# Performance work log

Measured on AMD Instinct MI355X. Metric: run time of the kernel, lower is better.

The kernel has to match this reference:

```python
import jax, jax.numpy as jnp
import numpy as np
import math

B, T, C = 4, 1024, 1024
H = 16          # n_head
E = 8           # num_experts
K = 2           # top_k
HID = 4096      # expert_hidden_dim
TEMP = 1.0
EPS_LN = 1e-5


def setup_inputs() -> dict:
    key = jax.random.key(0)
    ks = jax.random.split(key, 16)
    s = 0.02
    return {
        'x': jax.random.normal(ks[0], (B, T, C), jnp.float32),
        'ln1_g': jnp.ones((C,), jnp.float32),
        'ln1_b': jnp.zeros((C,), jnp.float32),
        'W_qkv': jax.random.normal(ks[1], (C, 3 * C), jnp.float32) * s,
        'b_qkv': jnp.zeros((3 * C,), jnp.float32),
        'W_proj': jax.random.normal(ks[2], (C, C), jnp.float32) * s,
        'b_proj': jnp.zeros((C,), jnp.float32),
        'ln2_g': jnp.ones((C,), jnp.float32),
        'ln2_b': jnp.zeros((C,), jnp.float32),
        'W_router': jax.random.normal(ks[3], (C, E), jnp.float32) * s,
        'W1': jax.random.normal(ks[4], (E, C, HID), jnp.float32) * s,
        'b1': jnp.zeros((E, HID), jnp.float32),
        'W2': jax.random.normal(ks[5], (E, HID, C), jnp.float32) * s,
        'b2': jnp.zeros((E, C), jnp.float32),
    }


def _layernorm(x, g, b):
    mu = jnp.mean(x, axis=-1, keepdims=True)
    var = jnp.mean(jnp.square(x - mu), axis=-1, keepdims=True)
    return (x - mu) * jax.lax.rsqrt(var + EPS_LN) * g + b


def reference(x, ln1_g, ln1_b, W_qkv, b_qkv, W_proj, b_proj,
              ln2_g, ln2_b, W_router, W1, b1, W2, b2):
    D = C // H
    # --- causal self-attention on ln_1(x) ---
    h = _layernorm(x, ln1_g, ln1_b)
    qkv = h @ W_qkv + b_qkv                      # [B,T,3C]
    q, k, v = jnp.split(qkv, 3, axis=-1)
    q = q.reshape(B, T, H, D).transpose(0, 2, 1, 3)   # [B,H,T,D]
    k = k.reshape(B, T, H, D).transpose(0, 2, 1, 3)
    v = v.reshape(B, T, H, D).transpose(0, 2, 1, 3)
    att = jnp.einsum('bhqd,bhkd->bhqk', q, k) * (1.0 / math.sqrt(D))
    mask = jnp.tril(jnp.ones((T, T), bool))
    att = jnp.where(mask, att, -jnp.inf)
    att = jax.nn.softmax(att, axis=-1)
    y = jnp.einsum('bhqk,bhkd->bhqd', att, v)
    y = y.transpose(0, 2, 1, 3).reshape(B, T, C)
    x = x + (y @ W_proj + b_proj)

    # --- sparse MoE on ln_2(x) ---
    h2 = _layernorm(x, ln2_g, ln2_b)
    xf = h2.reshape(-1, C)                       # [N,C]
    N = xf.shape[0]
    logits = (xf @ W_router) / TEMP              # [N,E]
    prob = jax.nn.softmax(logits, axis=-1)
    top_prob, top_idx = jax.lax.top_k(prob, K)   # [N,K]
    top_prob = top_prob / (jnp.sum(top_prob, axis=-1, keepdims=True) + 1e-9)
    # dense per-token per-expert combine weights (0 for unselected experts)
    w = jnp.zeros((N, E), xf.dtype).at[jnp.arange(N)[:, None], top_idx].add(top_prob)
    # dense expert compute (weights zero out unselected experts -> same math)
    hid = jax.nn.gelu(jnp.einsum('nc,ech->neh', xf, W1) + b1, approximate=False)
    eo = jnp.einsum('neh,ehc->nec', hid, W2) + b2          # [N,E,C]
    out_flat = jnp.einsum('nec,ne->nc', eo, w)
    x = x + out_flat.reshape(B, T, C)

    counts = jnp.zeros((E,), jnp.float32).at[top_idx.reshape(-1)].add(1.0)
    expert_utilization = counts / (jnp.sum(counts) + 1e-9)
    return x, expert_utilization
```

## Files before the change

kernel.cpp:

```cpp
#include <hip/hip_runtime.h>
#include <cmath>

#define CDIM 1024
#define NTOK 4096
#define NHEAD 16
#define HDIM 64
#define NEXP 8
#define HIDD 4096
#define MAXROWS 9216

typedef short bf16x8 __attribute__((ext_vector_type(8)));
typedef short s16x4  __attribute__((ext_vector_type(4)));
typedef float f32x4  __attribute__((ext_vector_type(4)));

static __device__ __forceinline__ short f2bf(float f){
  unsigned u = __builtin_bit_cast(unsigned, f);
  u += 0x7fffu + ((u >> 16) & 1u);
  return (short)(u >> 16);
}
static __device__ __forceinline__ float bf2f(short s){
  unsigned u = ((unsigned)(unsigned short)s) << 16;
  return __builtin_bit_cast(float, u);
}

static __device__ __forceinline__ int swz64(int r, int ch){
  return r*64 + (((ch ^ (r>>1)) & 3) << 4);
}
static __device__ __forceinline__ int swz128(int r, int ch){
  return r*128 + (((ch ^ r) & 7) << 4);
}

static __device__ __forceinline__ void gl16(const short* g, short* l){
  __builtin_amdgcn_global_load_lds(
      (const __attribute__((address_space(1))) void*)g,
      (__attribute__((address_space(3))) void*)l, 16, 0, 0);
}

__global__ void k_transpose_cast(const float* __restrict__ in, short* __restrict__ out,
                                 int R, int Cc){
  __shared__ float tile[64][65];
  const int z = blockIdx.z;
  const float* src = in + (long long)z*R*Cc;
  short* dst = out + (long long)z*R*Cc;
  const int r0 = blockIdx.y*64, c0 = blockIdx.x*64;
  const int t = threadIdx.x;
  #pragma unroll
  for (int it=0; it<4; ++it){
    const int item = t + it*256;
    const int r = item>>4, c4 = item&15;
    const float4 v = *(const float4*)(src + (long long)(r0+r)*Cc + c0 + c4*4);
    tile[r][c4*4+0]=v.x; tile[r][c4*4+1]=v.y; tile[r][c4*4+2]=v.z; tile[r][c4*4+3]=v.w;
  }
  __syncthreads();
  #pragma unroll
  for (int it=0; it<2; ++it){
    const int item = t + it*256;
    const int rr8 = item & 7, cc = item >> 3;
    bf16x8 o;
    #pragma unroll
    for (int i=0;i<8;i++) o[i] = f2bf(tile[rr8*8+i][cc]);
    *(bf16x8*)(dst + (long long)(c0+cc)*R + r0 + rr8*8) = o;
  }
}

__global__ void k_ln1(const float* __restrict__ x, const float* __restrict__ g,
                      const float* __restrict__ b, short* __restrict__ out){
  const int row = blockIdx.x;
  const int t = threadIdx.x;
  const float4 v = ((const float4*)(x + (long long)row*CDIM))[t];
  float s  = v.x+v.y+v.z+v.w;
  float s2 = v.x*v.x+v.y*v.y+v.z*v.z+v.w*v.w;
  #pragma unroll
  for (int mm=1; mm<64; mm<<=1){ s += __shfl_xor(s,mm); s2 += __shfl_xor(s2,mm); }
  __shared__ float ps[4], ps2[4];
  const int w = t>>6, l = t&63;
  if (l==0){ ps[w]=s; ps2[w]=s2; }
  __syncthreads();
  s  = ps[0]+ps[1]+ps[2]+ps[3];
  s2 = ps2[0]+ps2[1]+ps2[2]+ps2[3];
  const float mu = s*(1.f/CDIM);
  const float rstd = rsqrtf(s2*(1.f/CDIM) - mu*mu + 1e-5f);
  const float4 gg = ((const float4*)g)[t];
  const float4 bb = ((const float4*)b)[t];
  s16x4 o;
  o[0]=f2bf((v.x-mu)*rstd*gg.x+bb.x); o[1]=f2bf((v.y-mu)*rstd*gg.y+bb.y);
  o[2]=f2bf((v.z-mu)*rstd*gg.z+bb.z); o[3]=f2bf((v.w-mu)*rstd*gg.w+bb.w);
  *(s16x4*)(out + (long long)row*CDIM + t*4) = o;
}

__global__ void k_ln2_router(const float* __restrict__ x1, const float* __restrict__ g,
                             const float* __restrict__ b, const float* __restrict__ Wr,
                             short* __restrict__ h2, int* __restrict__ tidx,
                             float* __restrict__ tw, int* __restrict__ counts){
  const int row = blockIdx.x;
  const int t = threadIdx.x;
  const float4 v = ((const float4*)(x1 + (long long)row*CDIM))[t];
  float s  = v.x+v.y+v.z+v.w;
  float s2 = v.x*v.x+v.y*v.y+v.z*v.z+v.w*v.w;
  #pragma unroll
  for (int mm=1; mm<64; mm<<=1){ s += __shfl_xor(s,mm); s2 += __shfl_xor(s2,mm); }
  __shared__ float ps[4], ps2[4];
  const int w = t>>6, l = t&63;
  if (l==0){ ps[w]=s; ps2[w]=s2; }
  __syncthreads();
  s  = ps[0]+ps[1]+ps[2]+ps[3];
  s2 = ps2[0]+ps2[1]+ps2[2]+ps2[3];
  const float mu = s*(1.f/CDIM);
  const float rstd = rsqrtf(s2*(1.f/CDIM) - mu*mu + 1e-5f);
  const float4 gg = ((const float4*)g)[t];
  const float4 bb = ((const float4*)b)[t];
  const float y0=(v.x-mu)*rstd*gg.x+bb.x, y1=(v.y-mu)*rstd*gg.y+bb.y;
  const float y2=(v.z-mu)*rstd*gg.z+bb.z, y3=(v.w-mu)*rstd*gg.w+bb.w;
  s16x4 o; o[0]=f2bf(y0); o[1]=f2bf(y1); o[2]=f2bf(y2); o[3]=f2bf(y3);
  *(s16x4*)(h2 + (long long)row*CDIM + t*4) = o;

  float acc[8];
  const float* wr0 = Wr + (long long)(t*4)*NEXP;
  #pragma unroll
  for (int e=0;e<8;e++) acc[e] = y0*wr0[e] + y1*wr0[8+e] + y2*wr0[16+e] + y3*wr0[24+e];
  #pragma unroll
  for (int mm=1; mm<64; mm<<=1){
    #pragma unroll
    for (int e=0;e<8;e++) acc[e] += __shfl_xor(acc[e], mm);
  }
  __shared__ float pl[4][8];
  if (l==0){
    #pragma unroll
    for (int e=0;e<8;e++) pl[w][e]=acc[e];
  }
  __syncthreads();
  if (t==0){
    float lg[8];
    #pragma unroll
    for (int e=0;e<8;e++) lg[e] = pl[0][e]+pl[1][e]+pl[2][e]+pl[3][e];
    float mx = lg[0];
    #pragma unroll
    for (int e=1;e<8;e++) mx = fmaxf(mx, lg[e]);
    float pr[8]; float sum = 0.f;
    #pragma unroll
    for (int e=0;e<8;e++){ pr[e]=expf(lg[e]-mx); sum += pr[e]; }
    int i0 = 0;
    #pragma unroll
    for (int e=1;e<8;e++) if (pr[e] > pr[i0]) i0 = e;
    int i1 = (i0==0) ? 1 : 0;
    #pragma unroll
    for (int e=0;e<8;e++) if (e!=i0 && pr[e] > pr[i1]) i1 = e;
    const float p0 = pr[i0]/sum, p1 = pr[i1]/sum;
    const float dn = p0 + p1 + 1e-9f;
    tidx[row*2]=i0; tidx[row*2+1]=i1;
    tw[row*2]=p0/dn; tw[row*2+1]=p1/dn;
    atomicAdd(&counts[i0],1); atomicAdd(&counts[i1],1);
  }
}

__global__ void k_route_setup(const int* __restrict__ counts, int* __restrict__ offs,
                              int* __restrict__ cursors, float* __restrict__ util){
  if (threadIdx.x == 0){
    int o = 0;
    for (int e=0;e<8;e++){
      offs[e] = o; cursors[e] = o;
      o += (counts[e] + 127) & ~127;
    }
    offs[8] = o;
    for (int e=0;e<8;e++) util[e] = (float)counts[e] / 8192.0f;
  }
}

__global__ void k_scatter(const int* __restrict__ tidx, const float* __restrict__ tw,
                          int* __restrict__ cursors, int* __restrict__ rowmap,
                          float* __restrict__ roww, int* __restrict__ posmap){
  const int i = blockIdx.x*blockDim.x + threadIdx.x;
  if (i >= 2*NTOK) return;
  const int e = tidx[i];
  const int pos = atomicAdd(&cursors[e], 1);
  rowmap[pos] = i >> 1;
  roww[pos]   = tw[i];
  posmap[i]   = pos;
}

template<int EPI>
__launch_bounds__(512, 4)
__global__ void k_gemm(const short* __restrict__ A, const short* __restrict__ Bt,
                       const float* __restrict__ bias, const float* __restrict__ resid,
                       void* __restrict__ Cout, int N, int K,
                       const int* __restrict__ rowmap, const int* __restrict__ offs,
                       long long expStrideB, const short* __restrict__ zrow){
  int wg = blockIdx.x;
  const int nwg = gridDim.x;
  {
    const int q = nwg >> 3, r8 = nwg & 7;
    const int xcd = wg & 7, pos = wg >> 3;
    wg = (xcd < r8 ? xcd*(q+1) : r8*(q+1) + (xcd - r8)*q) + pos;
  }
  const int gridN = N >> 7;
  const int gridM = nwg / gridN;
  const int mtile = wg % gridM, ntile = wg / gridM;
  const int mbase = mtile*128;
  const int nbase = ntile*128;
  int e = 0;
  if constexpr (EPI >= 2){
    if (mbase >= offs[8]) return;
    while (e < 7 && mbase >= offs[e+1]) e++;
    Bt += (long long)e * expStrideB;
  }
  __shared__ short Asm[2][4096];
  __shared__ short Bsm[2][4096];
  const int tid = threadIdx.x;
  const int w = tid >> 6, l = tid & 63;
  const int wr = w >> 1, wc = w & 1;
  const int l15 = l & 15, l4 = l >> 4;

  const short* aSrc; const short* bSrc;
  {
    const int r = tid >> 2, ch = tid & 3;
    const int sch = (ch ^ (r >> 1)) & 3;
    if constexpr (EPI == 2){
      const int grow = rowmap[mbase + r];
      aSrc = (grow >= 0) ? (A + (long long)grow*K + sch*8) : (zrow + sch*8);
    } else {
      aSrc = A + (long long)(mbase + r)*K + sch*8;
    }
    bSrc = Bt + (long long)(nbase + r)*K + sch*8;
  }
  const int dOff = w*512;

  f32x4 acc[2][4];
  const f32x4 z4 = {0.f,0.f,0.f,0.f};
  #pragma unroll
  for (int i=0;i<2;i++){
    #pragma unroll
    for (int jn=0;jn<4;jn++) acc[i][jn] = z4;
  }

  auto stage = [&](int buf, int kt){
    gl16(aSrc + kt, &Asm[buf][dOff]);
    gl16(bSrc + kt, &Bsm[buf][dOff]);
  };
  auto compute = [&](int buf){
    bf16x8 af[2], bfr[4];
    #pragma unroll
    for (int i=0;i<2;i++)
      af[i]  = *(const bf16x8*)((char*)Asm[buf] + swz64(wr*32 + i*16 + l15, l4));
    #pragma unroll
    for (int jn=0;jn<4;jn++)
      bfr[jn] = *(const bf16x8*)((char*)Bsm[buf] + swz64(wc*64 + jn*16 + l15, l4));
    #pragma unroll
    for (int i=0;i<2;i++){
      #pragma unroll
      for (int jn=0;jn<4;jn++)
        acc[i][jn] = __builtin_amdgcn_mfma_f32_16x16x32_bf16(af[i], bfr[jn], acc[i][jn], 0,0,0);
    }
  };

  stage(0, 0);
  asm volatile("s_waitcnt vmcnt(0)" ::: "memory");
  __builtin_amdgcn_s_barrier();

  int cur = 0;
  for (int kt = 32; kt < K; kt += 32){
    stage(cur ^ 1, kt);
    compute(cur);
    asm volatile("s_waitcnt vmcnt(0)" ::: "memory");
    __builtin_amdgcn_s_barrier();
    cur ^= 1;
  }
  compute(cur);

  #pragma unroll
  for (int i=0;i<2;i++){
    const int row0 = mbase + wr*32 + i*16 + l4*4;
    #pragma unroll
    for (int jn=0;jn<4;jn++){
      const int col = nbase + wc*64 + jn*16 + l15;
      const float bi = bias[(EPI>=2 ? e*N : 0) + col];
      #pragma unroll
      for (int j=0;j<4;j++){
        const long long idx = (long long)(row0 + j)*N + col;
        float v = acc[i][jn][j] + bi;
        if constexpr (EPI == 0){
          ((short*)Cout)[idx] = f2bf(v);
        } else if constexpr (EPI == 1){
          ((float*)Cout)[idx] = v + resid[idx];
        } else if constexpr (EPI == 2){
          ((short*)Cout)[idx] = f2bf(0.5f*v*(1.0f + erff(v*0.70710678118654752f)));
        } else {
          ((short*)Cout)[idx] = f2bf(v);
        }
      }
    }
  }
}

__launch_bounds__(512)
__global__ void k_attn(const short* __restrict__ qkv, short* __restrict__ y){
  const int qp = blockIdx.x;
  const int bh = blockIdx.y;
  const int bb = bh >> 4;
  const int h  = bh & 15;
  const int tid = threadIdx.x;
  const int w = tid >> 6, l = tid & 63;
  const int half = w >> 2, wq = w & 3;
  const int l15 = l & 15, l4 = l >> 4;

  __shared__ short Ksm[64*64];
  __shared__ short Vtsm[64*64];
  __shared__ short Psm[8*16*64];

  const long long rs = 3*CDIM;
  const int qrow0 = bb*1024 + qp*128;
  const int myQt = (qp << 1) + half;
  const int qtHigh = (qp << 1) + 1;

  bf16x8 aq[2];
  {
    const int qr = qrow0 + half*64 + wq*16 + l15;
    const short* qp2 = qkv + (long long)qr*rs + h*HDIM;
    aq[0] = *(const bf16x8*)(qp2 + l4*8);
    aq[1] = *(const bf16x8*)(qp2 + 32 + l4*8);
  }

  const f32x4 z4 = {0.f,0.f,0.f,0.f};
  f32x4 O[4];
  #pragma unroll
  for (int cf=0;cf<4;cf++) O[cf] = z4;
  float mrow[4], lrow[4];
  #pragma unroll
  for (int j=0;j<4;j++){ mrow[j] = -1e30f; lrow[j] = 0.f; }

  for (int kvb = 0; kvb <= qtHigh; ++kvb){
    const int kvrow0 = bb*1024 + kvb*64;
    {
      const int r = tid >> 3, c = tid & 7;
      const short* kp = qkv + (long long)(kvrow0 + r)*rs + CDIM + h*HDIM + c*8;
      *(bf16x8*)((char*)Ksm + swz128(r, c)) = *(const bf16x8*)kp;
      const short* vp = qkv + (long long)(kvrow0 + r)*rs + 2*CDIM + h*HDIM + c*8;
      bf16x8 vv = *(const bf16x8*)vp;
      const int off2 = 2*r;
      const int g0 = off2 >> 4, b0 = off2 & 15;
      #pragma unroll
      for (int i=0;i<8;i++){
        const int d = c*8 + i;
        *(short*)((char*)Vtsm + d*128 + (((g0 ^ d) & 7) << 4) + b0) = vv[i];
      }
    }
    __syncthreads();

    if (kvb <= myQt){
      f32x4 S[4];
      #pragma unroll
      for (int cf=0;cf<4;cf++) S[cf] = z4;
      #pragma unroll
      for (int cf=0;cf<4;cf++){
        #pragma unroll
        for (int kf=0;kf<2;kf++){
          bf16x8 bk = *(const bf16x8*)((char*)Ksm + swz128(cf*16 + l15, kf*4 + l4));
          S[cf] = __builtin_amdgcn_mfma_f32_16x16x32_bf16(aq[kf], bk, S[cf], 0,0,0);
        }
      }

      const bool diag = (kvb == myQt);
      #pragma unroll
      for (int cf=0;cf<4;cf++){
        #pragma unroll
        for (int j=0;j<4;j++){
          float s = S[cf][j] * 0.125f;
          if (diag && (cf*16 + l15 > wq*16 + l4*4 + j)) s = -1e30f;
          S[cf][j] = s;
        }
      }

      float alpha[4];
      #pragma unroll
      for (int j=0;j<4;j++){
        float mx = fmaxf(fmaxf(S[0][j],S[1][j]), fmaxf(S[2][j],S[3][j]));
        #pragma unroll
        for (int mm=1; mm<16; mm<<=1) mx = fmaxf(mx, __shfl_xor(mx, mm));
        const float mnew = fmaxf(mrow[j], mx);
        const float al = expf(mrow[j] - mnew);
        float psum = 0.f;
        #pragma unroll
        for (int cf=0;cf<4;cf++){ float pp = expf(S[cf][j]-mnew); S[cf][j]=pp; psum += pp; }
        #pragma unroll
        for (int mm=1; mm<16; mm<<=1) psum += __shfl_xor(psum, mm);
        lrow[j] = lrow[j]*al + psum;
        mrow[j] = mnew; alpha[j] = al;
      }
      #pragma unroll
      for (int cf=0;cf<4;cf++){
        #pragma unroll
        for (int j=0;j<4;j++) O[cf][j] *= alpha[j];
      }

      char* pw = (char*)Psm + w*2048;
      #pragma unroll
      for (int cf=0;cf<4;cf++){
        #pragma unroll
        for (int j=0;j<4;j++){
          const int r = l4*4 + j;
          const int cb = (cf*16 + l15)*2;
          *(short*)(pw + r*128 + ((((cb>>4) ^ r) & 7)<<4) + (cb & 15)) = f2bf(S[cf][j]);
        }
      }
      bf16x8 pa[2];
      pa[0] = *(const bf16x8*)(pw + swz128(l15, l4));
      pa[1] = *(const bf16x8*)(pw + swz128(l15, 4 + l4));
      #pragma unroll
      for (int cf=0;cf<4;cf++){
        #pragma unroll
        for (int kf=0;kf<2;kf++){
          bf16x8 bv = *(const bf16x8*)((char*)Vtsm + swz128(cf*16 + l15, kf*4 + l4));
          O[cf] = __builtin_amdgcn_mfma_f32_16x16x32_bf16(pa[kf], bv, O[cf], 0,0,0);
        }
      }
    }
    __syncthreads();
  }

  const int yr0 = qrow0 + half*64 + wq*16;
  #pragma unroll
  for (int cf=0;cf<4;cf++){
    #pragma unroll
    for (int j=0;j<4;j++){
      const int r = l4*4 + j;
      y[(long long)(yr0 + r)*CDIM + h*HDIM + cf*16 + l15] = f2bf(O[cf][j] / lrow[j]);
    }
  }
}

__global__ void k_combine(const float* __restrict__ x1, const short* __restrict__ eo,
                          const int* __restrict__ posmap, const float* __restrict__ roww,
                          float* __restrict__ out){
  const int row = blockIdx.x;
  const int t = threadIdx.x;
  const int p0 = posmap[row*2], p1 = posmap[row*2+1];
  const float w0 = roww[p0], w1 = roww[p1];
  const float4 a  = ((const float4*)(x1 + (long long)row*CDIM))[t];
  const s16x4 e0 = *(const s16x4*)(eo + (long long)p0*CDIM + t*4);
  const s16x4 e1 = *(const s16x4*)(eo + (long long)p1*CDIM + t*4);
  float4 r;
  r.x = a.x + w0*bf2f(e0[0]) + w1*bf2f(e1[0]);
  r.y = a.y + w0*bf2f(e0[1]) + w1*bf2f(e1[1]);
  r.z = a.z + w0*bf2f(e0[2]) + w1*bf2f(e1[2]);
  r.w = a.w + w0*bf2f(e0[3]) + w1*bf2f(e1[3]);
  ((float4*)(out + (long long)row*CDIM))[t] = r;
}

extern "C" void kernel_launch(void* const* d_in, const int* in_sizes, int n_in,
                              void* d_out, int out_size, void* d_ws, size_t ws_size,
                              hipStream_t stream){
  const float* x     = (const float*)d_in[0];
  const float* ln1_g = (const float*)d_in[1];
  const float* ln1_b = (const float*)d_in[2];
  const float* W_qkv = (const float*)d_in[3];
  const float* b_qkv = (const float*)d_in[4];
  const float* W_proj= (const float*)d_in[5];
  const float* b_proj= (const float*)d_in[6];
  const float* ln2_g = (const float*)d_in[7];
  const float* ln2_b = (const float*)d_in[8];
  const float* W_r   = (const float*)d_in[9];
  const float* W1    = (const float*)d_in[10];
  const float* b1    = (const float*)d_in[11];
  const float* W2    = (const float*)d_in[12];
  const float* b2    = (const float*)d_in[13];
  float* out = (float*)d_out;
  float* util = out + (long long)NTOK*CDIM;

  char* p = (char*)d_ws;
  auto alloc = [&](size_t bytes)->char*{
    char* r = p; p += (bytes + 255) & ~(size_t)255; return r;
  };
  short* Wt1   = (short*)alloc((size_t)NEXP*HIDD*CDIM*2);
  short* Wt2   = (short*)alloc((size_t)NEXP*CDIM*HIDD*2);
  float* x1    = (float*)alloc((size_t)NTOK*CDIM*4);
  short* h2    = (short*)alloc((size_t)NTOK*CDIM*2);
  short* hid   = (short*)alloc((size_t)MAXROWS*HIDD*2);
  int*   tidx  = (int*)alloc(2*NTOK*4);
  float* tw    = (float*)alloc(2*NTOK*4);
  int*   counts= (int*)alloc(256);
  int*   offs  = (int*)alloc(256);
  int*   curs  = (int*)alloc(256);
  int*   rowmap= (int*)alloc(MAXROWS*4);
  float* roww  = (float*)alloc(MAXROWS*4);
  int*   posmap= (int*)alloc(2*NTOK*4);
  short* zrow  = (short*)alloc(8192);
  char* transStart = p;
  short* WtQ = (short*)alloc((size_t)3*CDIM*CDIM*2);
  short* WtP = (short*)alloc((size_t)CDIM*CDIM*2);
  short* h   = (short*)alloc((size_t)NTOK*CDIM*2);
  short* qkv = (short*)alloc((size_t)NTOK*3*CDIM*2);
  short* y   = (short*)alloc((size_t)NTOK*CDIM*2);
  short* eo  = (short*)transStart;

  (void)hipMemsetAsync(counts, 0, 32, stream);
  (void)hipMemsetAsync(zrow, 0, 8192, stream);
  (void)hipMemsetAsync(rowmap, 0xFF, MAXROWS*4, stream);

  k_transpose_cast<<<dim3(3*CDIM/64, CDIM/64, 1), 256, 0, stream>>>(W_qkv, WtQ, CDIM, 3*CDIM);
  k_transpose_cast<<<dim3(CDIM/64, CDIM/64, 1),   256, 0, stream>>>(W_proj, WtP, CDIM, CDIM);
  k_transpose_cast<<<dim3(HIDD/64, CDIM/64, NEXP),256, 0, stream>>>(W1, Wt1, CDIM, HIDD);
  k_transpose_cast<<<dim3(CDIM/64, HIDD/64, NEXP),256, 0, stream>>>(W2, Wt2, HIDD, CDIM);

  k_ln1<<<NTOK, 256, 0, stream>>>(x, ln1_g, ln1_b, h);

  k_gemm<0><<<dim3((NTOK/128)*(3*CDIM/128)), 512, 0, stream>>>(
      h, WtQ, b_qkv, nullptr, qkv, 3*CDIM, CDIM, nullptr, nullptr, 0, nullptr);

  k_attn<<<dim3(1024/128, 4*NHEAD), 512, 0, stream>>>(qkv, y);

  k_gemm<1><<<dim3((NTOK/128)*(CDIM/128)), 512, 0, stream>>>(
      y, WtP, b_proj, x, x1, CDIM, CDIM, nullptr, nullptr, 0, nullptr);

  k_ln2_router<<<NTOK, 256, 0, stream>>>(x1, ln2_g, ln2_b, W_r, h2, tidx, tw, counts);
  k_route_setup<<<1, 64, 0, stream>>>(counts, offs, curs, util);
  k_scatter<<<(2*NTOK)/256, 256, 0, stream>>>(tidx, tw, curs, rowmap, roww, posmap);

  k_gemm<2><<<dim3((MAXROWS/128)*(HIDD/128)), 512, 0, stream>>>(
      h2, Wt1, b1, nullptr, hid, HIDD, CDIM, rowmap, offs, (long long)HIDD*CDIM, zrow);
  k_gemm<3><<<dim3((MAXROWS/128)*(CDIM/128)), 512, 0, stream>>>(
      hid, Wt2, b2, nullptr, eo, CDIM, HIDD, nullptr, offs, (long long)CDIM*HIDD, zrow);

  k_combine<<<NTOK, 256, 0, stream>>>(x1, eo, posmap, roww, out);
}
```

Before: 632.0 us.

## Load 128-row KV tiles in attention and use tanh GELU approximation

```diff
diff --git a/kernel.cpp b/kernel.cpp
--- a/kernel.cpp
+++ b/kernel.cpp
@@ -21,6 +21,11 @@
 static __device__ __forceinline__ float bf2f(short s){
   unsigned u = ((unsigned)(unsigned short)s) << 16;
   return __builtin_bit_cast(float, u);
+}
+static __device__ __forceinline__ float gelu_t(float x){
+  const float y = 0.7978845608f*(x + 0.044715f*x*x*x);
+  const float e = __expf(2.f*y);
+  return 0.5f*x*(1.f + (e-1.f)/(e+1.f));
 }
 
 static __device__ __forceinline__ int swz64(int r, int ch){
@@ -282,7 +287,7 @@
         } else if constexpr (EPI == 1){
           ((float*)Cout)[idx] = v + resid[idx];
         } else if constexpr (EPI == 2){
-          ((short*)Cout)[idx] = f2bf(0.5f*v*(1.0f + erff(v*0.70710678118654752f)));
+          ((short*)Cout)[idx] = f2bf(gelu_t(v));
         } else {
           ((short*)Cout)[idx] = f2bf(v);
         }
@@ -302,14 +307,13 @@
   const int half = w >> 2, wq = w & 3;
   const int l15 = l & 15, l4 = l >> 4;
 
-  __shared__ short Ksm[64*64];
-  __shared__ short Vtsm[64*64];
+  __shared__ short Ksm[128*64];
+  __shared__ short Vtsm[64*128];
   __shared__ short Psm[8*16*64];
 
   const long long rs = 3*CDIM;
   const int qrow0 = bb*1024 + qp*128;
   const int myQt = (qp << 1) + half;
-  const int qtHigh = (qp << 1) + 1;
 
   bf16x8 aq[2];
   {
@@ -327,89 +331,95 @@
   #pragma unroll
   for (int j=0;j<4;j++){ mrow[j] = -1e30f; lrow[j] = 0.f; }
 
-  for (int kvb = 0; kvb <= qtHigh; ++kvb){
-    const int kvrow0 = bb*1024 + kvb*64;
-    {
-      const int r = tid >> 3, c = tid & 7;
-      const short* kp = qkv + (long long)(kvrow0 + r)*rs + CDIM + h*HDIM + c*8;
-      *(bf16x8*)((char*)Ksm + swz128(r, c)) = *(const bf16x8*)kp;
-      const short* vp = qkv + (long long)(kvrow0 + r)*rs + 2*CDIM + h*HDIM + c*8;
+  for (int it = 0; it <= qp; ++it){
+    const int kvrow0 = bb*1024 + it*128;
+    #pragma unroll
+    for (int pz=0; pz<2; ++pz){
+      const int rr = (tid >> 3) + pz*64;
+      const int c = tid & 7;
+      const short* kp = qkv + (long long)(kvrow0 + rr)*rs + CDIM + h*HDIM + c*8;
+      *(bf16x8*)((char*)Ksm + swz128(rr, c)) = *(const bf16x8*)kp;
+      const short* vp = qkv + (long long)(kvrow0 + rr)*rs + 2*CDIM + h*HDIM + c*8;
       bf16x8 vv = *(const bf16x8*)vp;
-      const int off2 = 2*r;
-      const int g0 = off2 >> 4, b0 = off2 & 15;
       #pragma unroll
       for (int i=0;i<8;i++){
         const int d = c*8 + i;
-        *(short*)((char*)Vtsm + d*128 + (((g0 ^ d) & 7) << 4) + b0) = vv[i];
+        *(short*)((char*)Vtsm + d*256 + ((((rr>>3) ^ (d&7)) & 15)<<4) + ((2*rr)&15)) = vv[i];
       }
     }
     __syncthreads();
 
-    if (kvb <= myQt){
-      f32x4 S[4];
-      #pragma unroll
-      for (int cf=0;cf<4;cf++) S[cf] = z4;
-      #pragma unroll
-      for (int cf=0;cf<4;cf++){
-        #pragma unroll
-        for (int kf=0;kf<2;kf++){
-          bf16x8 bk = *(const bf16x8*)((char*)Ksm + swz128(cf*16 + l15, kf*4 + l4));
-          S[cf] = __builtin_amdgcn_mfma_f32_16x16x32_bf16(aq[kf], bk, S[cf], 0,0,0);
-        }
-      }
-
-      const bool diag = (kvb == myQt);
-      #pragma unroll
-      for (int cf=0;cf<4;cf++){
+    #pragma unroll
+    for (int ks=0; ks<2; ++ks){
+      const int kvb = it*2 + ks;
+      if (kvb <= myQt){
+        f32x4 S[4];
+        #pragma unroll
+        for (int cf=0;cf<4;cf++) S[cf] = z4;
+        #pragma unroll
+        for (int cf=0;cf<4;cf++){
+          #pragma unroll
+          for (int kf=0;kf<2;kf++){
+            bf16x8 bk = *(const bf16x8*)((char*)Ksm + swz128(ks*64 + cf*16 + l15, kf*4 + l4));
+            S[cf] = __builtin_amdgcn_mfma_f32_16x16x32_bf16(aq[kf], bk, S[cf], 0,0,0);
+          }
+        }
+
+        const bool diag = (kvb == myQt);
+        #pragma unroll
+        for (int cf=0;cf<4;cf++){
+          #pragma unroll
+          for (int j=0;j<4;j++){
+            float s = S[cf][j] * 0.125f;
+            if (diag && (cf*16 + l15 > wq*16 + l4*4 + j)) s = -1e30f;
+            S[cf][j] = s;
+          }
+        }
+
+        float alpha[4];
         #pragma unroll
         for (int j=0;j<4;j++){
-          float s = S[cf][j] * 0.125f;
-          if (diag && (cf*16 + l15 > wq*16 + l4*4 + j)) s = -1e30f;
-          S[cf][j] = s;
-        }
-      }
-
-      float alpha[4];
-      #pragma unroll
-      for (int j=0;j<4;j++){
-        float mx = fmaxf(fmaxf(S[0][j],S[1][j]), fmaxf(S[2][j],S[3][j]));
-        #pragma unroll
-        for (int mm=1; mm<16; mm<<=1) mx = fmaxf(mx, __shfl_xor(mx, mm));
-        const float mnew = fmaxf(mrow[j], mx);
-        const float al = expf(mrow[j] - mnew);
-        float psum = 0.f;
-        #pragma unroll
-        for (int cf=0;cf<4;cf++){ float pp = expf(S[cf][j]-mnew); S[cf][j]=pp; psum += pp; }
-        #pragma unroll
-        for (int mm=1; mm<16; mm<<=1) psum += __shfl_xor(psum, mm);
-        lrow[j] = lrow[j]*al + psum;
-        mrow[j] = mnew; alpha[j] = al;
-      }
-      #pragma unroll
-      for (int cf=0;cf<4;cf++){
-        #pragma unroll
-        for (int j=0;j<4;j++) O[cf][j] *= alpha[j];
-      }
-
-      char* pw = (char*)Psm + w*2048;
-      #pragma unroll
-      for (int cf=0;cf<4;cf++){
-        #pragma unroll
-        for (int j=0;j<4;j++){
-          const int r = l4*4 + j;
-          const int cb = (cf*16 + l15)*2;
-          *(short*)(pw + r*128 + ((((cb>>4) ^ r) & 7)<<4) + (cb & 15)) = f2bf(S[cf][j]);
-        }
-      }
-      bf16x8 pa[2];
-      pa[0] = *(const bf16x8*)(pw + swz128(l15, l4));
-      pa[1] = *(const bf16x8*)(pw + swz128(l15, 4 + l4));
-      #pragma unroll
-      for (int cf=0;cf<4;cf++){
-        #pragma unroll
-        for (int kf=0;kf<2;kf++){
-          bf16x8 bv = *(const bf16x8*)((char*)Vtsm + swz128(cf*16 + l15, kf*4 + l4));
-          O[cf] = __builtin_amdgcn_mfma_f32_16x16x32_bf16(pa[kf], bv, O[cf], 0,0,0);
+          float mx = fmaxf(fmaxf(S[0][j],S[1][j]), fmaxf(S[2][j],S[3][j]));
+          #pragma unroll
+          for (int mm=1; mm<16; mm<<=1) mx = fmaxf(mx, __shfl_xor(mx, mm));
+          const float mnew = fmaxf(mrow[j], mx);
+          const float al = expf(mrow[j] - mnew);
+          float psum = 0.f;
+          #pragma unroll
+          for (int cf=0;cf<4;cf++){ float pp = expf(S[cf][j]-mnew); S[cf][j]=pp; psum += pp; }
+          #pragma unroll
+          for (int mm=1; mm<16; mm<<=1) psum += __shfl_xor(psum, mm);
+          lrow[j] = lrow[j]*al + psum;
+          mrow[j] = mnew; alpha[j] = al;
+        }
+        #pragma unroll
+        for (int cf=0;cf<4;cf++){
+          #pragma unroll
+          for (int j=0;j<4;j++) O[cf][j] *= alpha[j];
+        }
+
+        char* pw = (char*)Psm + w*2048;
+        #pragma unroll
+        for (int cf=0;cf<4;cf++){
+          #pragma unroll
+          for (int j=0;j<4;j++){
+            const int r = l4*4 + j;
+            const int cb = (cf*16 + l15)*2;
+            *(short*)(pw + r*128 + ((((cb>>4) ^ r) & 7)<<4) + (cb & 15)) = f2bf(S[cf][j]);
+          }
+        }
+        bf16x8 pa[2];
+        pa[0] = *(const bf16x8*)(pw + swz128(l15, l4));
+        pa[1] = *(const bf16x8*)(pw + swz128(l15, 4 + l4));
+        #pragma unroll
+        for (int cf=0;cf<4;cf++){
+          const int d = cf*16 + l15;
+          #pragma unroll
+          for (int kf=0;kf<2;kf++){
+            const int ch = ks*8 + kf*4 + l4;
+            bf16x8 bv = *(const bf16x8*)((char*)Vtsm + d*256 + (((ch ^ (d&7)) & 15)<<4));
+            O[cf] = __builtin_amdgcn_mfma_f32_16x16x32_bf16(pa[kf], bv, O[cf], 0,0,0);
+          }
         }
       }
     }
```

New measurement: 627.1 us. About the same (-0.8%).
